# Kernel optimization log

Measured on AMD Instinct MI355X. Metric: run time of the kernel, lower is better.

## Reference

```python
import jax, jax.numpy as jnp
import numpy as np

B, N, M, NF = 8, 512, 100, 42
DIMS = [NF, 256, 128, 64, 1]


def setup_inputs() -> dict:
    key = jax.random.key(0)
    ks = jax.random.split(key, 3 + len(DIMS) - 1)
    inp = {
        "image": jax.random.normal(ks[0], (B, N, NF), jnp.float32),
        "dfeat": jax.random.normal(ks[1], (B, N, M, NF, 3), jnp.float32) * 0.1,
        "neighbor": jax.random.randint(ks[2], (B, N, M), 0, N + 1),  # 0 = no neighbor, else 1-based atom idx
    }
    for l in range(len(DIMS) - 1):
        inp[f"W{l}"] = jax.random.normal(ks[3 + l], (DIMS[l], DIMS[l + 1]), jnp.float32) / np.sqrt(DIMS[l])
        inp[f"b{l}"] = jnp.zeros((DIMS[l + 1],), jnp.float32)
    return inp


def _atom_energy(x, Ws, bs):
    # per-atom MLP: sigmoid hidden layers, linear scalar output
    h = x
    for W, b in zip(Ws[:-1], bs[:-1]):
        h = jax.nn.sigmoid(h @ W + b)
    return (h @ Ws[-1] + bs[-1])[0]


def reference(image, dfeat, neighbor, W0, b0, W1, b1, W2, b2, W3, b3):
    Ws = (W0, W1, W2, W3)
    bs = (b0, b1, b2, b3)
    nb, na, nf = image.shape

    e_fn = lambda x: _atom_energy(x, Ws, bs)
    flat = image.reshape(-1, nf)
    Ei = jax.vmap(e_fn)(flat).reshape(nb, na)                      # [B, N]
    dE = jax.vmap(jax.grad(e_fn))(flat).reshape(nb, na, nf)        # dEi/dFeat, [B, N, F]
    Etot = jnp.sum(Ei, axis=1, keepdims=True)                      # [B, 1]

    # Force[b,i,:] = sum_m dE[b, neighbor[b,i,m]-1, :] @ dfeat[b,i,m,:,:], masking pad (0) entries
    mask = (neighbor > 0).astype(dE.dtype)                         # [B, N, M]
    idx = jnp.maximum(neighbor - 1, 0)                             # [B, N, M]
    dE_g = jax.vmap(lambda d, i: d[i])(dE, idx)                    # [B, N, M, F]
    Force = jnp.einsum('bnmf,bnmfd->bnd', dE_g * mask[..., None], dfeat)  # [B, N, 3]
    return Etot, Ei, Force
```

## Files before the change

### kernel.cpp

```cpp
#include <hip/hip_runtime.h>

#define NFEAT 42
#define H1 256
#define H2 128
#define H3 64
#define NB 8
#define NA 512
#define NM 100
#define TA 4

__device__ __forceinline__ float sigmoidf(float z) {
    return 1.0f / (1.0f + __expf(-z));
}

__global__ __launch_bounds__(256) void transpose_weights(
    const float* __restrict__ W0, const float* __restrict__ W1, const float* __restrict__ W2,
    float* __restrict__ W0T, float* __restrict__ W1T, float* __restrict__ W2T)
{
    int i = blockIdx.x * 256 + threadIdx.x;
    if (i < NFEAT * H1) {
        int f = i / H1, k = i - f * H1;
        W0T[k * NFEAT + f] = W0[i];
    }
    if (i < H1 * H2) {
        int k = i / H2, j = i - k * H2;
        W1T[j * H1 + k] = W1[i];
    }
    if (i < H2 * H3) {
        int j = i / H3, k = i - j * H3;
        W2T[k * H2 + j] = W2[i];
    }
}

__global__ __launch_bounds__(256) void mlp_fwd_bwd(
    const float* __restrict__ image,
    const float* __restrict__ W0, const float* __restrict__ b0,
    const float* __restrict__ W1, const float* __restrict__ b1,
    const float* __restrict__ W2, const float* __restrict__ b2,
    const float* __restrict__ W3, const float* __restrict__ b3,
    const float* __restrict__ W0T, const float* __restrict__ W1T, const float* __restrict__ W2T,
    float* __restrict__ Ei,
    float* __restrict__ dE)
{
    const int t = threadIdx.x;
    const int atom0 = blockIdx.x * TA;

    __shared__ float sx[TA][NFEAT];
    __shared__ __align__(16) float sh1[TA][H1];
    __shared__ __align__(16) float sh2[TA][H2];
    __shared__ __align__(16) float sh3[TA][H3];
    __shared__ __align__(16) float sd3[TA][H3];
    __shared__ __align__(16) float sd2[TA][H2];
    __shared__ __align__(16) float sd1[TA][H1];

    for (int i = t; i < TA * NFEAT; i += 256) {
        int a = i / NFEAT, f = i - a * NFEAT;
        sx[a][f] = image[(atom0 + a) * NFEAT + f];
    }
    __syncthreads();

    {
        float acc[TA] = {0.f, 0.f, 0.f, 0.f};
        for (int k = 0; k < NFEAT; ++k) {
            float w = W0[k * H1 + t];
            #pragma unroll
            for (int a = 0; a < TA; ++a) acc[a] += sx[a][k] * w;
        }
        float bb = b0[t];
        #pragma unroll
        for (int a = 0; a < TA; ++a) sh1[a][t] = sigmoidf(acc[a] + bb);
    }
    __syncthreads();

    {
        const int j = t & 127, a0 = (t >> 7) * 2;
        float acc[2] = {0.f, 0.f};
        for (int kk = 0; kk < H1 / 4; ++kk) {
            float w0_ = W1[(4 * kk + 0) * H2 + j];
            float w1_ = W1[(4 * kk + 1) * H2 + j];
            float w2_ = W1[(4 * kk + 2) * H2 + j];
            float w3_ = W1[(4 * kk + 3) * H2 + j];
            #pragma unroll
            for (int a = 0; a < 2; ++a) {
                float4 h = ((const float4*)sh1[a0 + a])[kk];
                acc[a] += h.x * w0_ + h.y * w1_ + h.z * w2_ + h.w * w3_;
            }
        }
        float bb = b1[j];
        #pragma unroll
        for (int a = 0; a < 2; ++a) sh2[a0 + a][j] = sigmoidf(acc[a] + bb);
    }
    __syncthreads();

    {
        const int j = t & 63, a = t >> 6;
        float acc = 0.f;
        for (int kk = 0; kk < H2 / 4; ++kk) {
            float w0_ = W2[(4 * kk + 0) * H3 + j];
            float w1_ = W2[(4 * kk + 1) * H3 + j];
            float w2_ = W2[(4 * kk + 2) * H3 + j];
            float w3_ = W2[(4 * kk + 3) * H3 + j];
            float4 h = ((const float4*)sh2[a])[kk];
            acc += h.x * w0_ + h.y * w1_ + h.z * w2_ + h.w * w3_;
        }
        sh3[a][j] = sigmoidf(acc + b2[j]);
    }
    __syncthreads();

    {
        const int lane = t & 63, a = t >> 6;
        float w = W3[lane];
        float bb = b3[0];
        float h = sh3[a][lane];
        sd3[a][lane] = w * h * (1.f - h);
        float v = w * h;
        #pragma unroll
        for (int off = 32; off > 0; off >>= 1) v += __shfl_down(v, off, 64);
        if (lane == 0) Ei[atom0 + a] = v + bb;
    }
    __syncthreads();

    {
        const int j = t & 127, a0 = (t >> 7) * 2;
        float acc[2] = {0.f, 0.f};
        for (int kk = 0; kk < H3 / 4; ++kk) {
            float w0_ = W2T[(4 * kk + 0) * H2 + j];
            float w1_ = W2T[(4 * kk + 1) * H2 + j];
            float w2_ = W2T[(4 * kk + 2) * H2 + j];
            float w3_ = W2T[(4 * kk + 3) * H2 + j];
            #pragma unroll
            for (int a = 0; a < 2; ++a) {
                float4 d = ((const float4*)sd3[a0 + a])[kk];
                acc[a] += d.x * w0_ + d.y * w1_ + d.z * w2_ + d.w * w3_;
            }
        }
        #pragma unroll
        for (int a = 0; a < 2; ++a) {
            float h = sh2[a0 + a][j];
            sd2[a0 + a][j] = acc[a] * h * (1.f - h);
        }
    }
    __syncthreads();

    {
        float acc[TA] = {0.f, 0.f, 0.f, 0.f};
        for (int jj = 0; jj < H2 / 4; ++jj) {
            float w0_ = W1T[(4 * jj + 0) * H1 + t];
            float w1_ = W1T[(4 * jj + 1) * H1 + t];
            float w2_ = W1T[(4 * jj + 2) * H1 + t];
            float w3_ = W1T[(4 * jj + 3) * H1 + t];
            #pragma unroll
            for (int a = 0; a < TA; ++a) {
                float4 d = ((const float4*)sd2[a])[jj];
                acc[a] += d.x * w0_ + d.y * w1_ + d.z * w2_ + d.w * w3_;
            }
        }
        #pragma unroll
        for (int a = 0; a < TA; ++a) {
            float h = sh1[a][t];
            sd1[a][t] = acc[a] * h * (1.f - h);
        }
    }
    __syncthreads();

    {
        const int f = t & 63, a = t >> 6;
        if (f < NFEAT) {
            float acc = 0.f;
            for (int kk = 0; kk < H1 / 4; ++kk) {
                float w0_ = W0T[(4 * kk + 0) * NFEAT + f];
                float w1_ = W0T[(4 * kk + 1) * NFEAT + f];
                float w2_ = W0T[(4 * kk + 2) * NFEAT + f];
                float w3_ = W0T[(4 * kk + 3) * NFEAT + f];
                float4 d = ((const float4*)sd1[a])[kk];
                acc += d.x * w0_ + d.y * w1_ + d.z * w2_ + d.w * w3_;
            }
            dE[(atom0 + a) * NFEAT + f] = acc;
        }
    }
}

__global__ __launch_bounds__(256) void etot_kernel(const float* __restrict__ Ei,
                                                   float* __restrict__ Etot)
{
    const int b = blockIdx.x;
    const int t = threadIdx.x;
    float v = Ei[b * NA + t] + Ei[b * NA + t + 256];
    __shared__ float red[4];
    #pragma unroll
    for (int off = 32; off > 0; off >>= 1) v += __shfl_down(v, off, 64);
    if ((t & 63) == 0) red[t >> 6] = v;
    __syncthreads();
    if (t == 0) Etot[b] = red[0] + red[1] + red[2] + red[3];
}

__global__ __launch_bounds__(256) void force_kernel(
    const float* __restrict__ dfeat,
    const int*   __restrict__ neighbor,
    const float* __restrict__ dE,
    float* __restrict__ Force)
{
    const int bi = blockIdx.x;
    const int b  = bi >> 9;
    const int t  = threadIdx.x;

    __shared__ int   s_nb[NM];
    __shared__ float s_dE[104 * NFEAT];
    __shared__ float s_part[1008];
    __shared__ float s_red[126];

    if (t < NM) s_nb[t] = neighbor[bi * NM + t];
    for (int i = t; i < 4 * NFEAT; i += 256) s_dE[NM * NFEAT + i] = 0.f;
    __syncthreads();

    for (int i = t; i < NM * NFEAT; i += 256) {
        int m = i / NFEAT, f = i - m * NFEAT;
        int n = s_nb[m];
        s_dE[i] = (n > 0) ? dE[((b << 9) + n - 1) * NFEAT + f] : 0.f;
    }
    __syncthreads();

    if (t < 252) {
        const int e4 = 4 * t;
        int off[4];
        #pragma unroll
        for (int c = 0; c < 4; ++c) {
            int ee = e4 + c;
            int r  = ee / 126;
            int e  = ee - r * 126;
            off[c] = r * NFEAT + e / 3;
        }
        const float* base = dfeat + (size_t)bi * (NM * NFEAT * 3);
        float acc[4] = {0.f, 0.f, 0.f, 0.f};

        for (int m0 = 0; m0 < 96; m0 += 8) {
            float4 v = *(const float4*)(base + m0 * 126 + e4);
            const float* sd = s_dE + m0 * NFEAT;
            acc[0] += v.x * sd[off[0]];
            acc[1] += v.y * sd[off[1]];
            acc[2] += v.z * sd[off[2]];
            acc[3] += v.w * sd[off[3]];
        }
        {
            const int m0 = 96;
            float vv[4];
            if (bi != NB * NA - 1) {
                float4 v = *(const float4*)(base + m0 * 126 + e4);
                vv[0] = v.x; vv[1] = v.y; vv[2] = v.z; vv[3] = v.w;
            } else {
                #pragma unroll
                for (int c = 0; c < 4; ++c) {
                    int r = (e4 + c) / 126;
                    vv[c] = (m0 + r < NM) ? base[m0 * 126 + e4 + c] : 0.f;
                }
            }
            const float* sd = s_dE + m0 * NFEAT;
            #pragma unroll
            for (int c = 0; c < 4; ++c) acc[c] += vv[c] * sd[off[c]];
        }
        #pragma unroll
        for (int c = 0; c < 4; ++c) s_part[e4 + c] = acc[c];
    }
    __syncthreads();

    if (t < 126) {
        float s = 0.f;
        #pragma unroll
        for (int r = 0; r < 8; ++r) s += s_part[r * 126 + t];
        s_red[t] = s;
    }
    __syncthreads();

    if (t < 3) {
        float s = 0.f;
        #pragma unroll
        for (int f = 0; f < NFEAT; ++f) s += s_red[f * 3 + t];
        Force[bi * 3 + t] = s;
    }
}

extern "C" void kernel_launch(void* const* d_in, const int* in_sizes, int n_in,
                              void* d_out, int out_size, void* d_ws, size_t ws_size,
                              hipStream_t stream) {
    const float* image    = (const float*)d_in[0];
    const float* dfeat    = (const float*)d_in[1];
    const int*   neighbor = (const int*)  d_in[2];
    const float* W0 = (const float*)d_in[3];
    const float* b0 = (const float*)d_in[4];
    const float* W1 = (const float*)d_in[5];
    const float* b1 = (const float*)d_in[6];
    const float* W2 = (const float*)d_in[7];
    const float* b2 = (const float*)d_in[8];
    const float* W3 = (const float*)d_in[9];
    const float* b3 = (const float*)d_in[10];

    float* out   = (float*)d_out;
    float* Etot  = out;
    float* Ei    = out + NB;
    float* Force = out + NB + NB * NA;

    float* dE  = (float*)d_ws;
    float* W0T = dE  + NB * NA * NFEAT;
    float* W1T = W0T + NFEAT * H1;
    float* W2T = W1T + H1 * H2;

    transpose_weights<<<(H1 * H2 + 255) / 256, 256, 0, stream>>>(W0, W1, W2, W0T, W1T, W2T);
    mlp_fwd_bwd<<<(NB * NA) / TA, 256, 0, stream>>>(image, W0, b0, W1, b1, W2, b2, W3, b3,
                                                    W0T, W1T, W2T, Ei, dE);
    etot_kernel<<<NB, 256, 0, stream>>>(Ei, Etot);
    force_kernel<<<NB * NA, 256, 0, stream>>>(dfeat, neighbor, dE, Force);
}
```

Baseline: 345.9 us.

## Remap MLP layer thread assignments to one atom per wave with two outputs per thread

```diff
diff --git a/kernel.cpp b/kernel.cpp
--- a/kernel.cpp
+++ b/kernel.cpp
@@ -1,6 +1,7 @@
 #include <hip/hip_runtime.h>
 
 #define NFEAT 42
+#define NF_PAD 44
 #define H1 256
 #define H2 128
 #define H3 64
@@ -45,7 +46,7 @@
     const int t = threadIdx.x;
     const int atom0 = blockIdx.x * TA;
 
-    __shared__ float sx[TA][NFEAT];
+    __shared__ __align__(16) float sx[TA][NF_PAD];
     __shared__ __align__(16) float sh1[TA][H1];
     __shared__ __align__(16) float sh2[TA][H2];
     __shared__ __align__(16) float sh3[TA][H3];
@@ -53,18 +54,31 @@
     __shared__ __align__(16) float sd2[TA][H2];
     __shared__ __align__(16) float sd1[TA][H1];
 
-    for (int i = t; i < TA * NFEAT; i += 256) {
-        int a = i / NFEAT, f = i - a * NFEAT;
-        sx[a][f] = image[(atom0 + a) * NFEAT + f];
+    for (int i = t; i < TA * NF_PAD; i += 256) {
+        int a = i / NF_PAD, f = i - a * NF_PAD;
+        sx[a][f] = (f < NFEAT) ? image[(atom0 + a) * NFEAT + f] : 0.f;
     }
     __syncthreads();
 
     {
         float acc[TA] = {0.f, 0.f, 0.f, 0.f};
-        for (int k = 0; k < NFEAT; ++k) {
-            float w = W0[k * H1 + t];
+        for (int c = 0; c < 10; ++c) {
+            float w0 = W0[(4 * c + 0) * H1 + t];
+            float w1 = W0[(4 * c + 1) * H1 + t];
+            float w2 = W0[(4 * c + 2) * H1 + t];
+            float w3 = W0[(4 * c + 3) * H1 + t];
             #pragma unroll
-            for (int a = 0; a < TA; ++a) acc[a] += sx[a][k] * w;
+            for (int a = 0; a < TA; ++a) {
+                float4 x = ((const float4*)sx[a])[c];
+                acc[a] += x.x * w0 + x.y * w1 + x.z * w2 + x.w * w3;
+            }
+        }
+        {
+            float w40 = W0[40 * H1 + t];
+            float w41 = W0[41 * H1 + t];
+            #pragma unroll
+            for (int a = 0; a < TA; ++a)
+                acc[a] += sx[a][40] * w40 + sx[a][41] * w41;
         }
         float bb = b0[t];
         #pragma unroll
@@ -73,37 +87,36 @@
     __syncthreads();
 
     {
-        const int j = t & 127, a0 = (t >> 7) * 2;
-        float acc[2] = {0.f, 0.f};
+        const int j0 = t & 63, j1 = j0 + 64, a = t >> 6;
+        float acc0 = 0.f, acc1 = 0.f;
         for (int kk = 0; kk < H1 / 4; ++kk) {
-            float w0_ = W1[(4 * kk + 0) * H2 + j];
-            float w1_ = W1[(4 * kk + 1) * H2 + j];
-            float w2_ = W1[(4 * kk + 2) * H2 + j];
-            float w3_ = W1[(4 * kk + 3) * H2 + j];
-            #pragma unroll
-            for (int a = 0; a < 2; ++a) {
-                float4 h = ((const float4*)sh1[a0 + a])[kk];
-                acc[a] += h.x * w0_ + h.y * w1_ + h.z * w2_ + h.w * w3_;
-            }
-        }
-        float bb = b1[j];
-        #pragma unroll
-        for (int a = 0; a < 2; ++a) sh2[a0 + a][j] = sigmoidf(acc[a] + bb);
-    }
-    __syncthreads();
-
-    {
-        const int j = t & 63, a = t >> 6;
-        float acc = 0.f;
+            float4 h = ((const float4*)sh1[a])[kk];
+            const float* w0r = W1 + (4 * kk + 0) * H2;
+            const float* w1r = W1 + (4 * kk + 1) * H2;
+            const float* w2r = W1 + (4 * kk + 2) * H2;
+            const float* w3r = W1 + (4 * kk + 3) * H2;
+            acc0 += h.x * w0r[j0] + h.y * w1r[j0] + h.z * w2r[j0] + h.w * w3r[j0];
+            acc1 += h.x * w0r[j1] + h.y * w1r[j1] + h.z * w2r[j1] + h.w * w3r[j1];
+        }
+        sh2[a][j0] = sigmoidf(acc0 + b1[j0]);
+        sh2[a][j1] = sigmoidf(acc1 + b1[j1]);
+    }
+    __syncthreads();
+
+    if (t < 128) {
+        const int j0 = t & 31, j1 = j0 + 32, a = t >> 5;
+        float acc0 = 0.f, acc1 = 0.f;
         for (int kk = 0; kk < H2 / 4; ++kk) {
-            float w0_ = W2[(4 * kk + 0) * H3 + j];
-            float w1_ = W2[(4 * kk + 1) * H3 + j];
-            float w2_ = W2[(4 * kk + 2) * H3 + j];
-            float w3_ = W2[(4 * kk + 3) * H3 + j];
             float4 h = ((const float4*)sh2[a])[kk];
-            acc += h.x * w0_ + h.y * w1_ + h.z * w2_ + h.w * w3_;
-        }
-        sh3[a][j] = sigmoidf(acc + b2[j]);
+            const float* w0r = W2 + (4 * kk + 0) * H3;
+            const float* w1r = W2 + (4 * kk + 1) * H3;
+            const float* w2r = W2 + (4 * kk + 2) * H3;
+            const float* w3r = W2 + (4 * kk + 3) * H3;
+            acc0 += h.x * w0r[j0] + h.y * w1r[j0] + h.z * w2r[j0] + h.w * w3r[j0];
+            acc1 += h.x * w0r[j1] + h.y * w1r[j1] + h.z * w2r[j1] + h.w * w3r[j1];
+        }
+        sh3[a][j0] = sigmoidf(acc0 + b2[j0]);
+        sh3[a][j1] = sigmoidf(acc1 + b2[j1]);
     }
     __syncthreads();
 
@@ -121,61 +134,67 @@
     __syncthreads();
 
     {
-        const int j = t & 127, a0 = (t >> 7) * 2;
-        float acc[2] = {0.f, 0.f};
+        const int j0 = t & 63, j1 = j0 + 64, a = t >> 6;
+        float acc0 = 0.f, acc1 = 0.f;
         for (int kk = 0; kk < H3 / 4; ++kk) {
-            float w0_ = W2T[(4 * kk + 0) * H2 + j];
-            float w1_ = W2T[(4 * kk + 1) * H2 + j];
-            float w2_ = W2T[(4 * kk + 2) * H2 + j];
-            float w3_ = W2T[(4 * kk + 3) * H2 + j];
-            #pragma unroll
-            for (int a = 0; a < 2; ++a) {
-                float4 d = ((const float4*)sd3[a0 + a])[kk];
-                acc[a] += d.x * w0_ + d.y * w1_ + d.z * w2_ + d.w * w3_;
+            float4 d = ((const float4*)sd3[a])[kk];
+            const float* w0r = W2T + (4 * kk + 0) * H2;
+            const float* w1r = W2T + (4 * kk + 1) * H2;
+            const float* w2r = W2T + (4 * kk + 2) * H2;
+            const float* w3r = W2T + (4 * kk + 3) * H2;
+            acc0 += d.x * w0r[j0] + d.y * w1r[j0] + d.z * w2r[j0] + d.w * w3r[j0];
+            acc1 += d.x * w0r[j1] + d.y * w1r[j1] + d.z * w2r[j1] + d.w * w3r[j1];
+        }
+        float h0 = sh2[a][j0];
+        float h1 = sh2[a][j1];
+        sd2[a][j0] = acc0 * h0 * (1.f - h0);
+        sd2[a][j1] = acc1 * h1 * (1.f - h1);
+    }
+    __syncthreads();
+
+    {
+        const int k0 = t & 127, k1 = k0 + 128, a0 = (t >> 7) * 2;
+        float accA0 = 0.f, accA1 = 0.f, accB0 = 0.f, accB1 = 0.f;
+        for (int jj = 0; jj < H2 / 4; ++jj) {
+            float4 dA = ((const float4*)sd2[a0])[jj];
+            float4 dB = ((const float4*)sd2[a0 + 1])[jj];
+            const float* w0r = W1T + (4 * jj + 0) * H1;
+            const float* w1r = W1T + (4 * jj + 1) * H1;
+            const float* w2r = W1T + (4 * jj + 2) * H1;
+            const float* w3r = W1T + (4 * jj + 3) * H1;
+            float w00 = w0r[k0], w01 = w0r[k1];
+            float w10 = w1r[k0], w11 = w1r[k1];
+            float w20 = w2r[k0], w21 = w2r[k1];
+            float w30 = w3r[k0], w31 = w3r[k1];
+            accA0 += dA.x * w00 + dA.y * w10 + dA.z * w20 + dA.w * w30;
+            accA1 += dA.x * w01 + dA.y * w11 + dA.z * w21 + dA.w * w31;
+            accB0 += dB.x * w00 + dB.y * w10 + dB.z * w20 + dB.w * w30;
+            accB1 += dB.x * w01 + dB.y * w11 + dB.z * w21 + dB.w * w31;
+        }
+        float h;
+        h = sh1[a0][k0];     sd1[a0][k0]     = accA0 * h * (1.f - h);
+        h = sh1[a0][k1];     sd1[a0][k1]     = accA1 * h * (1.f - h);
+        h = sh1[a0 + 1][k0]; sd1[a0 + 1][k0] = accB0 * h * (1.f - h);
+        h = sh1[a0 + 1][k1]; sd1[a0 + 1][k1] = accB1 * h * (1.f - h);
+    }
+    __syncthreads();
+
+    if (t < 128) {
+        const int f0 = t & 31, a = t >> 5;
+        if (f0 < 21) {
+            const int f1 = f0 + 21;
+            float acc0 = 0.f, acc1 = 0.f;
+            for (int kk = 0; kk < H1 / 4; ++kk) {
+                float4 d = ((const float4*)sd1[a])[kk];
+                const float* w0r = W0T + (4 * kk + 0) * NFEAT;
+                const float* w1r = W0T + (4 * kk + 1) * NFEAT;
+                const float* w2r = W0T + (4 * kk + 2) * NFEAT;
+                const float* w3r = W0T + (4 * kk + 3) * NFEAT;
+                acc0 += d.x * w0r[f0] + d.y * w1r[f0] + d.z * w2r[f0] + d.w * w3r[f0];
+                acc1 += d.x * w0r[f1] + d.y * w1r[f1] + d.z * w2r[f1] + d.w * w3r[f1];
             }
-        }
-        #pragma unroll
-        for (int a = 0; a < 2; ++a) {
-            float h = sh2[a0 + a][j];
-            sd2[a0 + a][j] = acc[a] * h * (1.f - h);
-        }
-    }
-    __syncthreads();
-
-    {
-        float acc[TA] = {0.f, 0.f, 0.f, 0.f};
-        for (int jj = 0; jj < H2 / 4; ++jj) {
-            float w0_ = W1T[(4 * jj + 0) * H1 + t];
-            float w1_ = W1T[(4 * jj + 1) * H1 + t];
-            float w2_ = W1T[(4 * jj + 2) * H1 + t];
-            float w3_ = W1T[(4 * jj + 3) * H1 + t];
-            #pragma unroll
-            for (int a = 0; a < TA; ++a) {
-                float4 d = ((const float4*)sd2[a])[jj];
-                acc[a] += d.x * w0_ + d.y * w1_ + d.z * w2_ + d.w * w3_;
-            }
-        }
-        #pragma unroll
-        for (int a = 0; a < TA; ++a) {
-            float h = sh1[a][t];
-            sd1[a][t] = acc[a] * h * (1.f - h);
-        }
-    }
-    __syncthreads();
-
-    {
-        const int f = t & 63, a = t >> 6;
-        if (f < NFEAT) {
-            float acc = 0.f;
-            for (int kk = 0; kk < H1 / 4; ++kk) {
-                float w0_ = W0T[(4 * kk + 0) * NFEAT + f];
-                float w1_ = W0T[(4 * kk + 1) * NFEAT + f];
-                float w2_ = W0T[(4 * kk + 2) * NFEAT + f];
-                float w3_ = W0T[(4 * kk + 3) * NFEAT + f];
-                float4 d = ((const float4*)sd1[a])[kk];
-                acc += d.x * w0_ + d.y * w1_ + d.z * w2_ + d.w * w3_;
-            }
-            dE[(atom0 + a) * NFEAT + f] = acc;
+            dE[(atom0 + a) * NFEAT + f0] = acc0;
+            dE[(atom0 + a) * NFEAT + f1] = acc1;
         }
     }
 }
```

New measurement: 355.9 us. 2.9% more time.
